# Kernel optimization log

Hardware: AMD Instinct MI355X
Metric: run time of the kernel (lower is better)

## Reference

```python
import jax, jax.numpy as jnp
import numpy as np

K = 32  # sae_k

def setup_inputs() -> dict:
    key = jax.random.key(0)
    k1, k2, k3 = jax.random.split(key, 3)
    B, D, H = 8192, 256, 8192  # batch, d_in, hidden_dim = d_in * scale_size
    x = jax.random.normal(k1, (B, D), dtype=jnp.float32)
    W_enc = jax.random.normal(k2, (H, D), dtype=jnp.float32) * (1.0 / np.sqrt(D))
    b_enc = jnp.zeros((H,), dtype=jnp.float32)
    # W_dec initialized as clone of encoder weight then row-normalized to unit norm
    W_dec = jax.random.normal(k3, (H, D), dtype=jnp.float32)
    W_dec = W_dec / (jnp.linalg.norm(W_dec, axis=1, keepdims=True) + jnp.finfo(jnp.float32).eps)
    b_dec = jnp.zeros((D,), dtype=jnp.float32)
    return {"x": x, "W_enc": W_enc, "b_enc": b_enc, "W_dec": W_dec, "b_dec": b_dec}

def reference(x, W_enc, b_enc, W_dec, b_dec):
    # sae_in = x - b_dec; pre_acts = relu(encoder(sae_in))
    sae_in = x - b_dec
    pre_acts = jax.nn.relu(jnp.einsum('bd,hd->bh', sae_in, W_enc) + b_enc)  # [B, H]
    # top-k activation: keep k largest latents per row, zero the rest
    topk_vals, topk_idx = jax.lax.top_k(pre_acts, K)  # [B, K]
    B = pre_acts.shape[0]
    rows = jnp.arange(B)[:, None]
    z = jnp.zeros_like(pre_acts).at[rows, topk_idx].set(topk_vals)  # sparse activation [B, H]
    # decode
    x_reconstructed = jnp.einsum('bh,hd->bd', z, W_dec) + b_dec
    return x_reconstructed
```

## Files before the change

### kernel.cpp

```cpp
#include <hip/hip_runtime.h>

#define DIN   256
#define HID   8192
#define BATCH 8192
#define TOPK  32
#define BM    64
#define HHALF 4096
#define NCH   16
#define NS1   48
#define MRG   96
#define NS2   40
#define AS_LD 264
#define XF_LD 260
#define CAP   112
#define K2_LD 113
#define WCAP  640
#define THRM  0.1375f
#define DBM   4
#define DT    256
#define GK_OFF ((size_t)4 << 20)

typedef __bf16 bf16x8 __attribute__((ext_vector_type(8)));
typedef unsigned short u16x8 __attribute__((ext_vector_type(8)));
typedef float f32x4v __attribute__((ext_vector_type(4)));

__device__ __forceinline__ unsigned short f2bf(float f) {
  unsigned x = __builtin_bit_cast(unsigned, f);
  x = x + 0x7fffu + ((x >> 16) & 1u);
  return (unsigned short)(x >> 16);
}

__global__ __launch_bounds__(512) void wenc_cast(
    const float* __restrict__ Wenc, unsigned short* __restrict__ wsb)
{
  const int g = (int)blockIdx.x * 512 + (int)threadIdx.x;
  const int h = g >> 5, u = g & 31, kg = u >> 2, quad = u & 3;
  const float* src = Wenc + (size_t)h * DIN + kg * 32 + quad * 8;
  float4 a = *(const float4*)src;
  float4 b = *(const float4*)(src + 4);
  u16x8 o;
  o[0] = f2bf(a.x); o[1] = f2bf(a.y); o[2] = f2bf(a.z); o[3] = f2bf(a.w);
  o[4] = f2bf(b.x); o[5] = f2bf(b.y); o[6] = f2bf(b.z); o[7] = f2bf(b.w);
  *(u16x8*)(wsb + ((size_t)(((h >> 4) * 8 + kg) * 64 + quad * 16 + (h & 15))) * 8) = o;
}

__global__ __launch_bounds__(512) void sae_enc(
    const float* __restrict__ x,    const float* __restrict__ benc,
    const float* __restrict__ bdec, const unsigned short* __restrict__ wsb,
    unsigned* __restrict__ gkeys)
{
  __shared__ __align__(16) union UA {
    unsigned short As[BM][AS_LD];
    struct { unsigned wkey[8][WCAP]; unsigned char wrow[8][WCAP]; } w;
  } ua;
  __shared__ unsigned keys2[BM][K2_LD];
  __shared__ int   cnt[BM];
  __shared__ float rthr[BM];
  __shared__ int   wn[8];

  const int tid  = (int)threadIdx.x;
  const int wave = tid >> 6;
  const int lane = tid & 63;
  const int quad = lane >> 4;
  const int ln15 = lane & 15;
  const int rt   = (int)blockIdx.x >> 1;
  const int hs   = (int)blockIdx.x & 1;
  const int mb   = rt * BM;

  #pragma unroll
  for (int u = 0; u < 2; ++u) {
    const int idx = u * 512 + tid;
    const int r = idx >> 4, seg = idx & 15;
    const float* xs = x + (size_t)(mb + r) * DIN + seg * 16;
    const float* bs = bdec + seg * 16;
    float ss = 0.0f;
    #pragma unroll
    for (int j = 0; j < 4; ++j) {
      float4 xv = *(const float4*)(xs + 4 * j);
      float4 bv = *(const float4*)(bs + 4 * j);
      float dx = xv.x - bv.x, dy = xv.y - bv.y;
      float dz = xv.z - bv.z, dw = xv.w - bv.w;
      ss += dx * dx + dy * dy + dz * dz + dw * dw;
      unsigned short* dst = &ua.As[r][seg * 16 + 4 * j];
      dst[0] = f2bf(dx); dst[1] = f2bf(dy);
      dst[2] = f2bf(dz); dst[3] = f2bf(dw);
    }
    #pragma unroll
    for (int d = 1; d < 16; d <<= 1) ss += __shfl_xor(ss, d, 16);
    if (seg == 0) { rthr[r] = THRM * sqrtf(ss); cnt[r] = 0; }
  }
  __syncthreads();

  bf16x8 afrag[4][8];
  #pragma unroll
  for (int mt = 0; mt < 4; ++mt)
    #pragma unroll
    for (int gk = 0; gk < 8; ++gk)
      afrag[mt][gk] = *(const bf16x8*)&ua.As[mt * 16 + ln15][gk * 32 + quad * 8];

  float thr[16];
  #pragma unroll
  for (int s = 0; s < 16; ++s) thr[s] = rthr[(s >> 2) * 16 + quad * 4 + (s & 3)];
  __syncthreads();

  unsigned wbase = 0;

  for (int c = 0; c < NCH; ++c) {
    const unsigned short* bp =
        wsb + (((size_t)(hs * 256 + c * 16 + wave * 2) * 512) + lane) * 8;
    #pragma unroll
    for (int nt = 0; nt < 2; ++nt) {
      bf16x8 bfrag[8];
      #pragma unroll
      for (int kg = 0; kg < 8; ++kg)
        bfrag[kg] = *(const bf16x8*)(bp + (size_t)nt * 4096 + (size_t)kg * 512);

      const int hcol = hs * HHALF + c * 256 + (wave * 2 + nt) * 16 + ln15;
      const float be = benc[hcol];
      f32x4v acc[4];
      #pragma unroll
      for (int mt = 0; mt < 4; ++mt)
        #pragma unroll
        for (int i = 0; i < 4; ++i) acc[mt][i] = be;

      #pragma unroll
      for (int kg = 0; kg < 8; ++kg)
        #pragma unroll
        for (int mt = 0; mt < 4; ++mt)
          acc[mt] = __builtin_amdgcn_mfma_f32_16x16x32_bf16(
              afrag[mt][kg], bfrag[kg], acc[mt], 0, 0, 0);

      const unsigned idxpart = (unsigned)(8191 - hcol);
      #pragma unroll
      for (int s = 0; s < 16; ++s) {
        const int mt = s >> 2, i = s & 3;
        const bool take = acc[mt][i] > thr[s];
        const unsigned long long bm = __ballot(take);
        if (take) {
          const int pos = (int)wbase + __popcll(bm & ((1ull << lane) - 1ull));
          if (pos < WCAP) {
            ua.w.wkey[wave][pos] = ((unsigned)f2bf(acc[mt][i]) << 16) | idxpart;
            ua.w.wrow[wave][pos] = (unsigned char)(mt * 16 + quad * 4 + i);
          }
        }
        wbase += (unsigned)__popcll(bm);
      }
    }
  }
  if (lane == 0) wn[wave] = (int)(wbase < WCAP ? wbase : WCAP);
  __syncthreads();

  for (int w = 0; w < 8; ++w) {
    const int n = wn[w];
    for (int e = tid; e < n; e += 512) {
      const unsigned k = ua.w.wkey[w][e];
      const int row = (int)ua.w.wrow[w][e];
      const int sl = atomicAdd(&cnt[row], 1);
      if (sl < CAP) keys2[row][sl] = k;
    }
  }
  __syncthreads();

  #pragma unroll
  for (int u = 0; u < 2; ++u) {
    const int row = u * 32 + (tid >> 4), l16 = tid & 15;
    const int n = min(cnt[row], CAP);
    unsigned myk[CAP / 16];
    int rk[CAP / 16];
    #pragma unroll
    for (int j = 0; j < CAP / 16; ++j) {
      const int idx = l16 + 16 * j;
      myk[j] = (idx < n) ? keys2[row][idx] : 0u;
      rk[j] = 0;
    }
    for (int e = 0; e < n; ++e) {
      const unsigned k2 = keys2[row][e];
      #pragma unroll
      for (int j = 0; j < CAP / 16; ++j) rk[j] += (k2 > myk[j]) ? 1 : 0;
    }
    unsigned* gout = gkeys + (size_t)(mb + row) * MRG + hs * NS1;
    #pragma unroll
    for (int j = 0; j < CAP / 16; ++j) {
      const int idx = l16 + 16 * j;
      if (idx < n && rk[j] < NS1) gout[rk[j]] = myk[j];
    }
    if (l16 == 0)
      for (int p = n; p < NS1; ++p) gout[p] = (unsigned)(0x4000 + hs * 64 + p);
  }
}

__global__ __launch_bounds__(DT) void sae_dec(
    const float* __restrict__ x,    const float* __restrict__ Wenc,
    const float* __restrict__ benc, const float* __restrict__ Wdec,
    const float* __restrict__ bdec, const unsigned* __restrict__ gkeys,
    float* __restrict__ out)
{
  __shared__ unsigned mk[DBM][MRG];
  __shared__ __align__(16) float xf[DBM][XF_LD];
  __shared__ float tv[DBM][NS2];
  __shared__ int   ti[DBM][NS2];
  __shared__ float sv[DBM][TOPK];
  __shared__ int   si[DBM][TOPK];

  const int tid = (int)threadIdx.x;
  const int mb  = (int)blockIdx.x * DBM;

  #pragma unroll
  for (int i = tid; i < DBM * MRG; i += DT)
    mk[i / MRG][i % MRG] = gkeys[(size_t)mb * MRG + i];

  {
    const int r = tid >> 6, seg = tid & 63;
    float4 xv = *(const float4*)(x + (size_t)(mb + r) * DIN + seg * 4);
    float4 bv = *(const float4*)(bdec + seg * 4);
    float4 d;
    d.x = xv.x - bv.x; d.y = xv.y - bv.y; d.z = xv.z - bv.z; d.w = xv.w - bv.w;
    *(float4*)&xf[r][seg * 4] = d;
  }
  __syncthreads();

  if (tid < DBM * 32) {
    const int row = tid >> 5, l32 = tid & 31;
    unsigned myk[3];
    int rk[3];
    #pragma unroll
    for (int j = 0; j < 3; ++j) { myk[j] = mk[row][l32 + 32 * j]; rk[j] = 0; }
    for (int e = 0; e < MRG; ++e) {
      const unsigned k2 = mk[row][e];
      #pragma unroll
      for (int j = 0; j < 3; ++j) rk[j] += (k2 > myk[j]) ? 1 : 0;
    }
    #pragma unroll
    for (int j = 0; j < 3; ++j)
      if (rk[j] < NS2) ti[row][rk[j]] = 8191 - (int)(myk[j] & 0xFFFFu);
  }
  __syncthreads();

  {
    const int sub = tid & 15, task = tid >> 4;
    for (int p = 0; p < (DBM * NS2) / 16; ++p) {
      const int pp = p * 16 + task;
      const int row = pp / NS2, cand = pp - row * NS2;
      const int h = ti[row][cand];
      double a0 = 0.0, a1 = 0.0;
      if (h >= 0) {
        const float* wp = Wenc + (size_t)h * DIN + sub * 16;
        const float* xp = &xf[row][sub * 16];
        float4 w0 = *(const float4*)(wp);
        float4 w1 = *(const float4*)(wp + 4);
        float4 w2 = *(const float4*)(wp + 8);
        float4 w3 = *(const float4*)(wp + 12);
        float4 x0 = *(const float4*)(xp);
        float4 x1 = *(const float4*)(xp + 4);
        float4 x2 = *(const float4*)(xp + 8);
        float4 x3 = *(const float4*)(xp + 12);
        a0 += (double)x0.x * (double)w0.x + (double)x0.y * (double)w0.y;
        a1 += (double)x0.z * (double)w0.z + (double)x0.w * (double)w0.w;
        a0 += (double)x1.x * (double)w1.x + (double)x1.y * (double)w1.y;
        a1 += (double)x1.z * (double)w1.z + (double)x1.w * (double)w1.w;
        a0 += (double)x2.x * (double)w2.x + (double)x2.y * (double)w2.y;
        a1 += (double)x2.z * (double)w2.z + (double)x2.w * (double)w2.w;
        a0 += (double)x3.x * (double)w3.x + (double)x3.y * (double)w3.y;
        a1 += (double)x3.z * (double)w3.z + (double)x3.w * (double)w3.w;
      }
      double accd = a0 + a1;
      accd += __shfl_xor(accd, 8, 16);
      accd += __shfl_xor(accd, 4, 16);
      accd += __shfl_xor(accd, 2, 16);
      accd += __shfl_xor(accd, 1, 16);
      if (sub == 0) {
        float ev = (h >= 0) ? ((float)accd + benc[h]) : 0.0f;
        ev = ev > 0.0f ? ev : 0.0f;
        tv[row][cand] = ev;
      }
    }
  }
  __syncthreads();

  if (tid < DBM * NS2) {
    const int row = tid / NS2, cand = tid - row * NS2;
    const float v = tv[row][cand];
    const int   h = ti[row][cand];
    int rk = 0;
    for (int e = 0; e < NS2; ++e) {
      const float v2 = tv[row][e];
      const int   h2 = ti[row][e];
      rk += (v2 > v || (v2 == v && (unsigned)h2 < (unsigned)h)) ? 1 : 0;
    }
    if (rk < TOPK) { sv[row][rk] = v; si[row][rk] = h; }
  }
  __syncthreads();

  {
    const int r = tid >> 6, d0 = (tid & 63) * 4;
    float4 bb = *(const float4*)(bdec + d0);
    float o0 = bb.x, o1 = bb.y, o2 = bb.z, o3 = bb.w;
    #pragma unroll
    for (int s = 0; s < TOPK; ++s) {
      const float v = sv[r][s];
      const int   h = si[r][s];
      const float* wp = Wdec + (size_t)((v > 0.0f) ? h : 0) * DIN + d0;
      float4 w = *(const float4*)wp;
      o0 += v * w.x; o1 += v * w.y; o2 += v * w.z; o3 += v * w.w;
    }
    float4 o;
    o.x = o0; o.y = o1; o.z = o2; o.w = o3;
    *(float4*)(out + (size_t)(mb + r) * DIN + d0) = o;
  }
}

extern "C" void kernel_launch(void* const* d_in, const int* in_sizes, int n_in,
                              void* d_out, int out_size, void* d_ws, size_t ws_size,
                              hipStream_t stream) {
  const float* x    = (const float*)d_in[0];
  const float* Wenc = (const float*)d_in[1];
  const float* benc = (const float*)d_in[2];
  const float* Wdec = (const float*)d_in[3];
  const float* bdec = (const float*)d_in[4];
  float* out = (float*)d_out;
  unsigned short* wsb = (unsigned short*)d_ws;
  unsigned* gkeys = (unsigned*)((char*)d_ws + GK_OFF);

  wenc_cast<<<dim3((HID * DIN / 8) / 512), dim3(512), 0, stream>>>(Wenc, wsb);
  sae_enc<<<dim3(2 * BATCH / BM), dim3(512), 0, stream>>>(x, benc, bdec, wsb, gkeys);
  sae_dec<<<dim3(BATCH / DBM), dim3(DT), 0, stream>>>(x, Wenc, benc, Wdec, bdec, gkeys, out);
}
```

Baseline: 211.7 us.

## Halve encoder row tile to 32 and stage encoder bias in LDS for occupancy

Shrinks the encoder block's row tile from 64 to 32 rows, cutting A-fragment, accumulator and threshold registers in half and shrinking the per-wave candidate buffer. It requests 4 waves per EU and preloads the half of b_enc the block needs into shared memory instead of reading it from global memory per tile. The intent is higher occupancy to hide latency, at the cost of twice as many blocks, each re-streaming the full bf16 weight half, which doubles weight traffic per output row. A smaller WCAP also raises the risk of dropping candidates.

```diff
diff --git a/kernel.cpp b/kernel.cpp
--- a/kernel.cpp
+++ b/kernel.cpp
@@ -4,7 +4,7 @@
 #define HID   8192
 #define BATCH 8192
 #define TOPK  32
-#define BM    64
+#define BM    32
 #define HHALF 4096
 #define NCH   16
 #define NS1   48
@@ -14,7 +14,7 @@
 #define XF_LD 260
 #define CAP   112
 #define K2_LD 113
-#define WCAP  640
+#define WCAP  352
 #define THRM  0.1375f
 #define DBM   4
 #define DT    256
@@ -44,7 +44,8 @@
   *(u16x8*)(wsb + ((size_t)(((h >> 4) * 8 + kg) * 64 + quad * 16 + (h & 15))) * 8) = o;
 }
 
-__global__ __launch_bounds__(512) void sae_enc(
+__global__ __launch_bounds__(512) __attribute__((amdgpu_waves_per_eu(4)))
+void sae_enc(
     const float* __restrict__ x,    const float* __restrict__ benc,
     const float* __restrict__ bdec, const unsigned short* __restrict__ wsb,
     unsigned* __restrict__ gkeys)
@@ -54,6 +55,7 @@
     struct { unsigned wkey[8][WCAP]; unsigned char wrow[8][WCAP]; } w;
   } ua;
   __shared__ unsigned keys2[BM][K2_LD];
+  __shared__ __align__(16) float benc_l[HHALF];
   __shared__ int   cnt[BM];
   __shared__ float rthr[BM];
   __shared__ int   wn[8];
@@ -67,10 +69,8 @@
   const int hs   = (int)blockIdx.x & 1;
   const int mb   = rt * BM;
 
-  #pragma unroll
-  for (int u = 0; u < 2; ++u) {
-    const int idx = u * 512 + tid;
-    const int r = idx >> 4, seg = idx & 15;
+  {
+    const int r = tid >> 4, seg = tid & 15;
     const float* xs = x + (size_t)(mb + r) * DIN + seg * 16;
     const float* bs = bdec + seg * 16;
     float ss = 0.0f;
@@ -89,18 +89,25 @@
     for (int d = 1; d < 16; d <<= 1) ss += __shfl_xor(ss, d, 16);
     if (seg == 0) { rthr[r] = THRM * sqrtf(ss); cnt[r] = 0; }
   }
-  __syncthreads();
-
-  bf16x8 afrag[4][8];
+  {
+    const float* bsrc = benc + hs * HHALF + tid * 8;
+    float4 b0 = *(const float4*)bsrc;
+    float4 b1 = *(const float4*)(bsrc + 4);
+    *(float4*)&benc_l[tid * 8]     = b0;
+    *(float4*)&benc_l[tid * 8 + 4] = b1;
+  }
+  __syncthreads();
+
+  bf16x8 afrag[2][8];
   #pragma unroll
-  for (int mt = 0; mt < 4; ++mt)
+  for (int mt = 0; mt < 2; ++mt)
     #pragma unroll
     for (int gk = 0; gk < 8; ++gk)
       afrag[mt][gk] = *(const bf16x8*)&ua.As[mt * 16 + ln15][gk * 32 + quad * 8];
 
-  float thr[16];
+  float thr[8];
   #pragma unroll
-  for (int s = 0; s < 16; ++s) thr[s] = rthr[(s >> 2) * 16 + quad * 4 + (s & 3)];
+  for (int s = 0; s < 8; ++s) thr[s] = rthr[(s >> 2) * 16 + quad * 4 + (s & 3)];
   __syncthreads();
 
   unsigned wbase = 0;
@@ -115,24 +122,23 @@
       for (int kg = 0; kg < 8; ++kg)
         bfrag[kg] = *(const bf16x8*)(bp + (size_t)nt * 4096 + (size_t)kg * 512);
 
-      const int hcol = hs * HHALF + c * 256 + (wave * 2 + nt) * 16 + ln15;
-      const float be = benc[hcol];
-      f32x4v acc[4];
-      #pragma unroll
-      for (int mt = 0; mt < 4; ++mt)
+      const int hwl = c * 256 + (wave * 2 + nt) * 16 + ln15;
+      const float be = benc_l[hwl];
+      f32x4v acc[2];
+      #pragma unroll
+      for (int mt = 0; mt < 2; ++mt)
         #pragma unroll
         for (int i = 0; i < 4; ++i) acc[mt][i] = be;
 
       #pragma unroll
-      for (int kg = 0; kg < 8; ++kg)
-        #pragma unroll
-        for (int mt = 0; mt < 4; ++mt)
-          acc[mt] = __builtin_amdgcn_mfma_f32_16x16x32_bf16(
-              afrag[mt][kg], bfrag[kg], acc[mt], 0, 0, 0);
-
-      const unsigned idxpart = (unsigned)(8191 - hcol);
-      #pragma unroll
-      for (int s = 0; s < 16; ++s) {
+      for (int kg = 0; kg < 8; ++kg) {
+        acc[0] = __builtin_amdgcn_mfma_f32_16x16x32_bf16(afrag[0][kg], bfrag[kg], acc[0], 0, 0, 0);
+        acc[1] = __builtin_amdgcn_mfma_f32_16x16x32_bf16(afrag[1][kg], bfrag[kg], acc[1], 0, 0, 0);
+      }
+
+      const unsigned idxpart = (unsigned)(8191 - (hs * HHALF + hwl));
+      #pragma unroll
+      for (int s = 0; s < 8; ++s) {
         const int mt = s >> 2, i = s & 3;
         const bool take = acc[mt][i] > thr[s];
         const unsigned long long bm = __ballot(take);
@@ -161,9 +167,8 @@
   }
   __syncthreads();
 
-  #pragma unroll
-  for (int u = 0; u < 2; ++u) {
-    const int row = u * 32 + (tid >> 4), l16 = tid & 15;
+  {
+    const int row = tid >> 4, l16 = tid & 15;
     const int n = min(cnt[row], CAP);
     unsigned myk[CAP / 16];
     int rk[CAP / 16];
```

Measured after the change: 197.2 us. 6.9% less time.
